# Kernel tuning notes

Measured on AMD Instinct MI355X. Metric: run time of the kernel, lower is better.

Reference implementation:

```python
import jax, jax.numpy as jnp
import numpy as np

B, S, C, H, W = 4, 32, 128, 16, 32
HID = 128
DEPTH = 2


def conv2d_same(x, w, b):
    # x: [B,Cin,H,W], w: [Cout,Cin,3,3] -> [B,Cout,H,W]
    y = jax.lax.conv_general_dilated(x, w, window_strides=(1, 1), padding='SAME',
                                     dimension_numbers=('NCHW', 'OIHW', 'NCHW'))
    return y + b[None, :, None, None]


def setup_inputs() -> dict:
    key = jax.random.key(0)
    ks = jax.random.split(key, 12)
    sc = 0.02
    x = jax.random.normal(ks[0], (B, S, C, H, W), dtype=jnp.float32)
    # stacked ConvLSTM cell params; input to each cell is C==HID channels
    conv_w = sc * jax.random.normal(ks[1], (DEPTH, 4 * HID, C + HID, 3, 3), dtype=jnp.float32)
    conv_b = jnp.zeros((DEPTH, 4 * HID), dtype=jnp.float32)
    init_h = 0.01 * jax.random.normal(ks[2], (DEPTH, HID), dtype=jnp.float32)
    init_c = 0.01 * jax.random.normal(ks[3], (DEPTH, HID), dtype=jnp.float32)
    fc_w = sc * jax.random.normal(ks[4], (C, HID), dtype=jnp.float32)
    fc_b = jnp.zeros((C,), dtype=jnp.float32)
    fco_w = sc * jax.random.normal(ks[5], (1, C), dtype=jnp.float32)
    fco_b = jnp.zeros((1,), dtype=jnp.float32)
    fca_w = sc * jax.random.normal(ks[6], (1, C), dtype=jnp.float32)
    fca_b = jnp.zeros((1,), dtype=jnp.float32)
    return dict(x=x, conv_w=conv_w, conv_b=conv_b, init_h=init_h, init_c=init_c,
                fc_w=fc_w, fc_b=fc_b, fco_w=fco_w, fco_b=fco_b, fca_w=fca_w, fca_b=fca_b)


def _forward(x, conv_w, conv_b, init_h, init_c, fc_w, fc_b, fco_w, fco_b, fca_w, fca_b):
    b, s, c, h, w = x.shape
    hid = init_h.shape[1]
    xs = jnp.moveaxis(x, 1, 0)  # [S,B,C,H,W] time-major for scan
    for d in range(conv_w.shape[0]):  # fixed small depth loop
        wd, bd = conv_w[d], conv_b[d]
        h0 = jnp.broadcast_to(init_h[d][None, :, None, None], (b, hid, h, w))
        c0 = jnp.broadcast_to(init_c[d][None, :, None, None], (b, hid, h, w))

        def step(carry, x_t):
            hs, cs = carry
            z = conv2d_same(jnp.concatenate([x_t, hs], axis=1), wd, bd)
            zi, zf, zg, zo = jnp.split(z, 4, axis=1)  # gate order i,f,g,o
            cs = jax.nn.sigmoid(zf) * cs + jax.nn.sigmoid(zi) * jnp.tanh(zg)
            hs = jax.nn.sigmoid(zo) * jnp.tanh(cs)
            return (hs, cs), hs

        _, xs = jax.lax.scan(step, (h0, c0), xs)
    # global average pool over H,W then heads
    feat = jnp.moveaxis(xs.mean(axis=(3, 4)), 0, 1)  # [B,S,HID]
    feat = jax.nn.relu(feat @ fc_w.T + fc_b)
    offset = feat @ fco_w.T + fco_b  # [B,S,1]
    angle = feat @ fca_w.T + fca_b   # [B,S,1]
    return offset, angle


def reference(x, conv_w, conv_b, init_h, init_c, fc_w, fc_b, fco_w, fco_b, fca_w, fca_b):
    return _forward(x, conv_w, conv_b, init_h, init_c, fc_w, fc_b, fco_w, fco_b, fca_w, fca_b)
```

## Files before the change

### kernel.cpp

```cpp
#include <hip/hip_runtime.h>

#define BB 4
#define SS 32
#define CC 128
#define HH 16
#define WW 32
#define HID 128
#define DEPTH 2
#define CIN 256
#define COUT 512
#define K9 (CIN * 9)
#define KH 1152
#define KFULL (2 * KH)
#define HW (HH * WW)
#define MM (BB * HW)
#define ACT (BB * HW * 128)

typedef __attribute__((ext_vector_type(4))) float f32x4;
typedef __attribute__((ext_vector_type(8))) short bf16x8;

static __device__ __forceinline__ unsigned short f2bf(float f) {
    union { float f; unsigned u; } v; v.f = f;
    unsigned r = v.u + 0x7FFF + ((v.u >> 16) & 1);
    return (unsigned short)(r >> 16);
}
static __device__ __forceinline__ float bf2f(unsigned short h) {
    union { float f; unsigned u; } v; v.u = ((unsigned)h) << 16; return v.f;
}

__global__ void transpose_w_kernel(const float* __restrict__ w,
                                   unsigned short* __restrict__ wh) {
    int idx = blockIdx.x * 256 + threadIdx.x;
    if (idx >= DEPTH * K9 * COUT) return;
    int n = idx % COUT;
    int k = (idx / COUT) % K9;
    int d = idx / (COUT * K9);
    int cin = k / 9, tap = k % 9;
    float v = w[(((long)(d * COUT + n) * CIN + cin) * 9) + tap];
    int row = (cin < CC) ? (tap * CC + cin) : (KH + tap * HID + (cin - CC));
    int g = n >> 7, r = n & 127;
    int ng = (r >> 4) * 64 + g * 16 + (r & 15);
    wh[((long)d * COUT + ng) * KFULL + row] = f2bf(v);
}

__global__ void pack_x_kernel(const float* __restrict__ x,
                              unsigned* __restrict__ xh32) {
    __shared__ unsigned lh[128 * 33];
    const int tid = threadIdx.x;
    const int sb  = blockIdx.x;
    const int s   = sb >> 2;
    const int b   = sb & 3;
    const int hw0 = blockIdx.y * 64;
    const float* src = x + ((long)(b * SS + s) * CC) * HW;

    #pragma unroll
    for (int it = 0; it < 16; ++it) {
        int cc = it * 8 + (tid >> 5);
        int hw = (tid & 31) * 2;
        float2 v = *(const float2*)&src[cc * HW + hw0 + hw];
        unsigned short h0 = f2bf(v.x), h1 = f2bf(v.y);
        lh[cc * 33 + (hw >> 1)] = (unsigned)h0 | ((unsigned)h1 << 16);
    }
    __syncthreads();
    const unsigned short* lhs = (const unsigned short*)lh;
    #pragma unroll
    for (int it = 0; it < 16; ++it) {
        int hw = it * 4 + (tid >> 6);
        int c2 = tid & 63;
        unsigned short a0 = lhs[(2 * c2) * 66 + hw];
        unsigned short a1 = lhs[(2 * c2 + 1) * 66 + hw];
        long o = ((long)sb * HW + hw0 + hw) * 64 + c2;
        xh32[o] = (unsigned)a0 | ((unsigned)a1 << 16);
    }
}

__global__ void init_state_kernel(const float* __restrict__ ih, const float* __restrict__ ic,
                                  unsigned short* __restrict__ hh,
                                  float* __restrict__ c, int d) {
    int idx = blockIdx.x * 256 + threadIdx.x;
    int hid = idx & 127;
    hh[idx] = f2bf(ih[d * HID + hid]);
    c[idx] = ic[d * HID + hid];
}

__global__ void zero_kernel(unsigned* __restrict__ zp) { zp[threadIdx.x] = 0u; }

__launch_bounds__(256)
__global__ void step_dual(
    const unsigned short* __restrict__ x1h, const unsigned short* __restrict__ h1h,
    float* __restrict__ c1, unsigned short* __restrict__ o1h,
    const unsigned short* __restrict__ x2h, const unsigned short* __restrict__ h2h,
    float* __restrict__ c2, unsigned short* __restrict__ o2h,
    const unsigned short* __restrict__ wh,
    const float* __restrict__ bias, const unsigned short* __restrict__ zp,
    int do1, int do2)
{
    __shared__ __align__(16) unsigned short lds[2][8192];

    const int bid  = blockIdx.x;
    const int xcd  = bid & 7;
    const int q    = bid >> 3;
    const int mblk = q & 31;
    const int pp   = xcd + ((q >> 5) << 3);
    const int nblk = pp & 7;
    const int z    = pp >> 3;
    if (z == 0) { if (!do1) return; } else { if (!do2) return; }

    const unsigned short* axh = z ? x2h : x1h;
    const unsigned short* ahh = z ? h2h : h1h;
    const unsigned short* wph = wh + (long)z * COUT * KFULL;
    const float* bsel  = bias + z * COUT;
    float* csel        = z ? c2 : c1;
    unsigned short* ohh = z ? o2h : o1h;

    const int m0   = mblk * 64;
    const int n0g  = nblk * 64;
    const int hid0 = nblk * 16;
    const int tid  = threadIdx.x;
    const int lane = tid & 63;
    const int wv   = tid >> 6;
    const int wm   = (wv >> 1) * 32;
    const int wn   = (wv & 1) * 32;
    const int b    = m0 >> 9;
    const int hwl  = m0 & 511;
    const int y0   = hwl >> 5;

    const int row1 = wv * 16 + (lane >> 3);
    const int row2 = row1 + 8;
    const int jch  = lane & 7;
    const int jx1  = jch ^ (row1 & 7);
    const int jx2  = jch ^ (row2 & 7);
    const int sx1  = row1 & 31, sy1b = row1 >> 5;
    const int sx2  = row2 & 31, sy2b = row2 >> 5;
    const long bhw = (long)b * HW;
    const long bro1 = (long)(n0g + row1) * KFULL + jx1 * 8;
    const long bro2 = (long)(n0g + row2) * KFULL + jx2 * 8;

#define ISSUE(tt, pb) do {                                                        \
        const int _tt = (tt);                                                     \
        const long _k0 = (long)_tt * 64;                                          \
        int _ks = (_tt < 18) ? _tt : _tt - 18;                                    \
        int _tap = _ks >> 1;                                                      \
        int _c0  = (_ks & 1) << 6;                                                \
        int _ky  = _tap / 3 - 1;                                                  \
        int _kx  = _tap - (_tap / 3) * 3 - 1;                                     \
        const unsigned short* _sh = (_tt < 18) ? axh : ahh;                       \
        int _y1 = y0 + sy1b + _ky, _x1 = sx1 + _kx;                               \
        int _y2 = y0 + sy2b + _ky, _x2 = sx2 + _kx;                               \
        bool _o1 = (unsigned)_y1 < (unsigned)HH && (unsigned)_x1 < (unsigned)WW;  \
        bool _o2 = (unsigned)_y2 < (unsigned)HH && (unsigned)_x2 < (unsigned)WW;  \
        long _a1 = ((bhw + _y1 * WW + _x1) << 7) + _c0 + jx1 * 8;                 \
        long _a2 = ((bhw + _y2 * WW + _x2) << 7) + _c0 + jx2 * 8;                 \
        __builtin_amdgcn_global_load_lds(                                         \
            (const unsigned int*)(_o1 ? _sh + _a1 : zp),                          \
            (unsigned int*)&lds[pb][wv * 1024], 16, 0, 0);                        \
        __builtin_amdgcn_global_load_lds(                                         \
            (const unsigned int*)(_o2 ? _sh + _a2 : zp),                          \
            (unsigned int*)&lds[pb][wv * 1024 + 512], 16, 0, 0);                  \
        __builtin_amdgcn_global_load_lds(                                         \
            (const unsigned int*)(wph + bro1 + _k0),                              \
            (unsigned int*)&lds[pb][4096 + wv * 1024], 16, 0, 0);                 \
        __builtin_amdgcn_global_load_lds(                                         \
            (const unsigned int*)(wph + bro2 + _k0),                              \
            (unsigned int*)&lds[pb][4096 + wv * 1024 + 512], 16, 0, 0);           \
    } while (0)

    f32x4 acc00 = (f32x4){0.f,0.f,0.f,0.f};
    f32x4 acc01 = (f32x4){0.f,0.f,0.f,0.f};
    f32x4 acc10 = (f32x4){0.f,0.f,0.f,0.f};
    f32x4 acc11 = (f32x4){0.f,0.f,0.f,0.f};

    const int fr  = lane & 15;
    const int kqi = lane >> 4;
    const int am0 = wm + fr;
    const int am1 = wm + 16 + fr;
    const int bn0 = wn + fr;
    const int bn1 = wn + 16 + fr;

#define COMPUTE(P) do {                                                                  \
        const unsigned short* L = &lds[P][0];                                            \
        __builtin_amdgcn_s_setprio(1);                                                   \
        _Pragma("unroll")                                                                \
        for (int s = 0; s < 2; ++s) {                                                    \
            const int ca = s * 4 + kqi;                                  \
            bf16x8 fa0 = *(const bf16x8*)&L[am0 * 64 + ((ca ^ (am0 & 7)) << 3)];         \
            bf16x8 fa1 = *(const bf16x8*)&L[am1 * 64 + ((ca ^ (am1 & 7)) << 3)];         \
            bf16x8 fb0 = *(const bf16x8*)&L[4096 + bn0 * 64 + ((ca ^ (bn0 & 7)) << 3)];  \
            bf16x8 fb1 = *(const bf16x8*)&L[4096 + bn1 * 64 + ((ca ^ (bn1 & 7)) << 3)];  \
            acc00 = __builtin_amdgcn_mfma_f32_16x16x32_bf16(fa0, fb0, acc00, 0, 0, 0);   \
            acc01 = __builtin_amdgcn_mfma_f32_16x16x32_bf16(fa0, fb1, acc01, 0, 0, 0);   \
            acc10 = __builtin_amdgcn_mfma_f32_16x16x32_bf16(fa1, fb0, acc10, 0, 0, 0);   \
            acc11 = __builtin_amdgcn_mfma_f32_16x16x32_bf16(fa1, fb1, acc11, 0, 0, 0);   \
        }                                                                                \
        __builtin_amdgcn_s_setprio(0);                                                   \
    } while (0)

    ISSUE(0, 0);
    __syncthreads();

    int p = 0;
    for (int tt = 0; tt < 36; ++tt) {
        if (tt + 1 < 36) ISSUE(tt + 1, 1 - p);
        COMPUTE(p);
        __syncthreads();
        p ^= 1;
    }

#undef ISSUE
#undef COMPUTE

    float* zt = (float*)&lds[0][0];
    {
        const int rm = (lane >> 4) * 4;
        const int cn = lane & 15;
        *(float4*)&zt[(wn + cn) * 68 + wm + rm]           = *(float4*)&acc00;
        *(float4*)&zt[(wn + 16 + cn) * 68 + wm + rm]      = *(float4*)&acc01;
        *(float4*)&zt[(wn + cn) * 68 + wm + 16 + rm]      = *(float4*)&acc10;
        *(float4*)&zt[(wn + 16 + cn) * 68 + wm + 16 + rm] = *(float4*)&acc11;
    }
    __syncthreads();

    #pragma unroll
    for (int i2 = 0; i2 < 4; ++i2) {
        int e  = i2 * 256 + tid;
        int m  = e & 63;
        int jh = e >> 6;
        float g4[4];
        #pragma unroll
        for (int gi = 0; gi < 4; ++gi)
            g4[gi] = zt[(gi * 16 + jh) * 68 + m] + bsel[gi * 128 + hid0 + jh];
        long idx = ((long)b * HW + hwl + m) * 128 + hid0 + jh;
        float si = 1.f / (1.f + expf(-g4[0]));
        float sf = 1.f / (1.f + expf(-g4[1]));
        float so = 1.f / (1.f + expf(-g4[3]));
        float cs = sf * csel[idx] + si * tanhf(g4[2]);
        float hs = so * tanhf(cs);
        csel[idx] = cs;
        ohh[idx] = f2bf(hs);
    }
}

__global__ void pool_kernel(const unsigned short* __restrict__ s2h,
                            float* __restrict__ pooled) {
    int bs = blockIdx.x;
    int j  = threadIdx.x;
    const unsigned short* ph = s2h + (long)bs * HW * 128 + j;
    float sum = 0.f;
    #pragma unroll 8
    for (int hw = 0; hw < HW; ++hw)
        sum += bf2f(ph[hw * 128]);
    pooled[bs * HID + j] = sum * (1.f / HW);
}

__global__ void head_kernel(const float* __restrict__ pooled,
                            const float* __restrict__ fc_w, const float* __restrict__ fc_b,
                            const float* __restrict__ fco_w, const float* __restrict__ fco_b,
                            const float* __restrict__ fca_w, const float* __restrict__ fca_b,
                            float* __restrict__ out) {
    int bs = blockIdx.x;
    int b  = bs / SS;
    int s  = bs % SS;
    int j  = threadIdx.x;
    const float* prow = pooled + (long)(s * BB + b) * HID;
    float acc = fc_b[j];
    #pragma unroll 4
    for (int k = 0; k < HID; ++k) acc += fc_w[j * HID + k] * prow[k];
    float f = fmaxf(acc, 0.f);
    __shared__ float ro[128], ra[128];
    ro[j] = f * fco_w[j];
    ra[j] = f * fca_w[j];
    __syncthreads();
    for (int off = 64; off; off >>= 1) {
        if (j < off) { ro[j] += ro[j + off]; ra[j] += ra[j + off]; }
        __syncthreads();
    }
    if (j == 0) {
        out[bs]           = ro[0] + fco_b[0];
        out[BB * SS + bs] = ra[0] + fca_b[0];
    }
}

extern "C" void kernel_launch(void* const* d_in, const int* in_sizes, int n_in,
                              void* d_out, int out_size, void* d_ws, size_t ws_size,
                              hipStream_t stream) {
    const float* x      = (const float*)d_in[0];
    const float* conv_w = (const float*)d_in[1];
    const float* conv_b = (const float*)d_in[2];
    const float* init_h = (const float*)d_in[3];
    const float* init_c = (const float*)d_in[4];
    const float* fc_w   = (const float*)d_in[5];
    const float* fc_b   = (const float*)d_in[6];
    const float* fco_w  = (const float*)d_in[7];
    const float* fco_b  = (const float*)d_in[8];
    const float* fca_w  = (const float*)d_in[9];
    const float* fca_b  = (const float*)d_in[10];
    float* out = (float*)d_out;

    unsigned short* wh  = (unsigned short*)d_ws;
    unsigned short* xph = wh  + (long)DEPTH * COUT * KFULL;
    unsigned short* s1h = xph + (long)SS * ACT;
    unsigned short* s2h = s1h + (long)SS * ACT;
    unsigned short* h1h = s2h + (long)SS * ACT;
    unsigned short* h2h = h1h + ACT;
    float* c1     = (float*)(h2h + ACT);
    float* c2     = c1 + ACT;
    float* pooled = c2 + ACT;
    unsigned short* zp = (unsigned short*)(pooled + SS * BB * HID);

    transpose_w_kernel<<<(DEPTH * K9 * COUT + 255) / 256, 256, 0, stream>>>(conv_w, wh);
    pack_x_kernel<<<dim3(SS * BB, HW / 64), 256, 0, stream>>>(x, (unsigned*)xph);
    init_state_kernel<<<ACT / 256, 256, 0, stream>>>(init_h, init_c, h1h, c1, 0);
    init_state_kernel<<<ACT / 256, 256, 0, stream>>>(init_h, init_c, h2h, c2, 1);
    zero_kernel<<<1, 64, 0, stream>>>((unsigned*)zp);

    for (int t = 0; t <= SS; ++t) {
        int do1 = (t < SS) ? 1 : 0;
        int do2 = (t >= 1) ? 1 : 0;
        int t1 = (t < SS) ? t : SS - 1;
        int u2 = (t >= 1) ? t - 1 : 0;
        const unsigned short* ax1h = xph + (long)t1 * ACT;
        const unsigned short* ah1h = (t1 == 0) ? h1h : s1h + (long)(t1 - 1) * ACT;
        unsigned short* ao1h = s1h + (long)t1 * ACT;
        const unsigned short* ax2h = s1h + (long)u2 * ACT;
        const unsigned short* ah2h = (u2 == 0) ? h2h : s2h + (long)(u2 - 1) * ACT;
        unsigned short* ao2h = s2h + (long)u2 * ACT;
        step_dual<<<512, 256, 0, stream>>>(
            ax1h, ah1h, c1, ao1h,
            ax2h, ah2h, c2, ao2h,
            wh, conv_b, zp, do1, do2);
    }

    pool_kernel<<<SS * BB, 128, 0, stream>>>(s2h, pooled);
    head_kernel<<<BB * SS, 128, 0, stream>>>(pooled, fc_w, fc_b, fco_w, fco_b, fca_w, fca_b, out);
}
```

Before: 862.9 us.

## Double K-tile depth to 128 and vectorize the gate epilogue stores

```diff
diff --git a/kernel.cpp b/kernel.cpp
--- a/kernel.cpp
+++ b/kernel.cpp
@@ -95,7 +95,7 @@
     const float* __restrict__ bias, const unsigned short* __restrict__ zp,
     int do1, int do2)
 {
-    __shared__ __align__(16) unsigned short lds[2][8192];
+    __shared__ __align__(16) unsigned short lds[2][16384];
 
     const int bid  = blockIdx.x;
     const int xcd  = bid & 7;
@@ -124,45 +124,39 @@
     const int b    = m0 >> 9;
     const int hwl  = m0 & 511;
     const int y0   = hwl >> 5;
-
-    const int row1 = wv * 16 + (lane >> 3);
-    const int row2 = row1 + 8;
-    const int jch  = lane & 7;
-    const int jx1  = jch ^ (row1 & 7);
-    const int jx2  = jch ^ (row2 & 7);
-    const int sx1  = row1 & 31, sy1b = row1 >> 5;
-    const int sx2  = row2 & 31, sy2b = row2 >> 5;
     const long bhw = (long)b * HW;
-    const long bro1 = (long)(n0g + row1) * KFULL + jx1 * 8;
-    const long bro2 = (long)(n0g + row2) * KFULL + jx2 * 8;
+
+    int sy_[4], sx_[4], ax_[4];
+    long bro_[4];
+    #pragma unroll
+    for (int s = 0; s < 4; ++s) {
+        int row = wv * 16 + s * 4 + (lane >> 4);
+        int jx  = (lane & 15) ^ (row & 7);
+        sx_[s] = row & 31;
+        sy_[s] = y0 + (row >> 5);
+        ax_[s] = jx * 8;
+        bro_[s] = (long)(n0g + row) * KFULL + jx * 8;
+    }
 
 #define ISSUE(tt, pb) do {                                                        \
         const int _tt = (tt);                                                     \
-        const long _k0 = (long)_tt * 64;                                          \
-        int _ks = (_tt < 18) ? _tt : _tt - 18;                                    \
-        int _tap = _ks >> 1;                                                      \
-        int _c0  = (_ks & 1) << 6;                                                \
-        int _ky  = _tap / 3 - 1;                                                  \
-        int _kx  = _tap - (_tap / 3) * 3 - 1;                                     \
-        const unsigned short* _sh = (_tt < 18) ? axh : ahh;                       \
-        int _y1 = y0 + sy1b + _ky, _x1 = sx1 + _kx;                               \
-        int _y2 = y0 + sy2b + _ky, _x2 = sx2 + _kx;                               \
-        bool _o1 = (unsigned)_y1 < (unsigned)HH && (unsigned)_x1 < (unsigned)WW;  \
-        bool _o2 = (unsigned)_y2 < (unsigned)HH && (unsigned)_x2 < (unsigned)WW;  \
-        long _a1 = ((bhw + _y1 * WW + _x1) << 7) + _c0 + jx1 * 8;                 \
-        long _a2 = ((bhw + _y2 * WW + _x2) << 7) + _c0 + jx2 * 8;                 \
-        __builtin_amdgcn_global_load_lds(                                         \
-            (const unsigned int*)(_o1 ? _sh + _a1 : zp),                          \
-            (unsigned int*)&lds[pb][wv * 1024], 16, 0, 0);                        \
-        __builtin_amdgcn_global_load_lds(                                         \
-            (const unsigned int*)(_o2 ? _sh + _a2 : zp),                          \
-            (unsigned int*)&lds[pb][wv * 1024 + 512], 16, 0, 0);                  \
-        __builtin_amdgcn_global_load_lds(                                         \
-            (const unsigned int*)(wph + bro1 + _k0),                              \
-            (unsigned int*)&lds[pb][4096 + wv * 1024], 16, 0, 0);                 \
-        __builtin_amdgcn_global_load_lds(                                         \
-            (const unsigned int*)(wph + bro2 + _k0),                              \
-            (unsigned int*)&lds[pb][4096 + wv * 1024 + 512], 16, 0, 0);           \
+        const int _tap = (_tt < 9) ? _tt : _tt - 9;                               \
+        const unsigned short* _sh = (_tt < 9) ? axh : ahh;                        \
+        const int _ky = _tap / 3 - 1;                                             \
+        const int _kx = _tap - (_tap / 3) * 3 - 1;                                \
+        const long _bk = (long)_tt * 128;                                         \
+        _Pragma("unroll")                                                         \
+        for (int _s = 0; _s < 4; ++_s) {                                          \
+            int _yy = sy_[_s] + _ky, _xq = sx_[_s] + _kx;                         \
+            bool _ok = (unsigned)_yy < (unsigned)HH && (unsigned)_xq < (unsigned)WW;\
+            long _a = ((bhw + _yy * WW + _xq) << 7) + ax_[_s];                    \
+            __builtin_amdgcn_global_load_lds(                                     \
+                (const unsigned int*)(_ok ? _sh + _a : zp),                       \
+                (unsigned int*)&lds[pb][wv * 2048 + _s * 512], 16, 0, 0);         \
+            __builtin_amdgcn_global_load_lds(                                     \
+                (const unsigned int*)(wph + bro_[_s] + _bk),                      \
+                (unsigned int*)&lds[pb][8192 + wv * 2048 + _s * 512], 16, 0, 0);  \
+        }                                                                         \
     } while (0)
 
     f32x4 acc00 = (f32x4){0.f,0.f,0.f,0.f};
@@ -177,30 +171,30 @@
     const int bn0 = wn + fr;
     const int bn1 = wn + 16 + fr;
 
-#define COMPUTE(P) do {                                                                  \
-        const unsigned short* L = &lds[P][0];                                            \
-        __builtin_amdgcn_s_setprio(1);                                                   \
-        _Pragma("unroll")                                                                \
-        for (int s = 0; s < 2; ++s) {                                                    \
-            const int ca = s * 4 + kqi;                                  \
-            bf16x8 fa0 = *(const bf16x8*)&L[am0 * 64 + ((ca ^ (am0 & 7)) << 3)];         \
-            bf16x8 fa1 = *(const bf16x8*)&L[am1 * 64 + ((ca ^ (am1 & 7)) << 3)];         \
-            bf16x8 fb0 = *(const bf16x8*)&L[4096 + bn0 * 64 + ((ca ^ (bn0 & 7)) << 3)];  \
-            bf16x8 fb1 = *(const bf16x8*)&L[4096 + bn1 * 64 + ((ca ^ (bn1 & 7)) << 3)];  \
-            acc00 = __builtin_amdgcn_mfma_f32_16x16x32_bf16(fa0, fb0, acc00, 0, 0, 0);   \
-            acc01 = __builtin_amdgcn_mfma_f32_16x16x32_bf16(fa0, fb1, acc01, 0, 0, 0);   \
-            acc10 = __builtin_amdgcn_mfma_f32_16x16x32_bf16(fa1, fb0, acc10, 0, 0, 0);   \
-            acc11 = __builtin_amdgcn_mfma_f32_16x16x32_bf16(fa1, fb1, acc11, 0, 0, 0);   \
-        }                                                                                \
-        __builtin_amdgcn_s_setprio(0);                                                   \
+#define COMPUTE(P) do {                                                                   \
+        const unsigned short* L = &lds[P][0];                                             \
+        __builtin_amdgcn_s_setprio(1);                                                    \
+        _Pragma("unroll")                                                                 \
+        for (int s2 = 0; s2 < 4; ++s2) {                                                  \
+            const int ca = s2 * 4 + kqi;                                 \
+            bf16x8 fa0 = *(const bf16x8*)&L[am0 * 128 + ((ca ^ (am0 & 7)) << 3)];         \
+            bf16x8 fa1 = *(const bf16x8*)&L[am1 * 128 + ((ca ^ (am1 & 7)) << 3)];         \
+            bf16x8 fb0 = *(const bf16x8*)&L[8192 + bn0 * 128 + ((ca ^ (bn0 & 7)) << 3)];  \
+            bf16x8 fb1 = *(const bf16x8*)&L[8192 + bn1 * 128 + ((ca ^ (bn1 & 7)) << 3)];  \
+            acc00 = __builtin_amdgcn_mfma_f32_16x16x32_bf16(fa0, fb0, acc00, 0, 0, 0);    \
+            acc01 = __builtin_amdgcn_mfma_f32_16x16x32_bf16(fa0, fb1, acc01, 0, 0, 0);    \
+            acc10 = __builtin_amdgcn_mfma_f32_16x16x32_bf16(fa1, fb0, acc10, 0, 0, 0);    \
+            acc11 = __builtin_amdgcn_mfma_f32_16x16x32_bf16(fa1, fb1, acc11, 0, 0, 0);    \
+        }                                                                                 \
+        __builtin_amdgcn_s_setprio(0);                                                    \
     } while (0)
 
     ISSUE(0, 0);
     __syncthreads();
 
     int p = 0;
-    for (int tt = 0; tt < 36; ++tt) {
-        if (tt + 1 < 36) ISSUE(tt + 1, 1 - p);
+    for (int tt = 0; tt < 18; ++tt) {
+        if (tt + 1 < 18) ISSUE(tt + 1, 1 - p);
         COMPUTE(p);
         __syncthreads();
         p ^= 1;
@@ -220,23 +214,34 @@
     }
     __syncthreads();
 
-    #pragma unroll
-    for (int i2 = 0; i2 < 4; ++i2) {
-        int e  = i2 * 256 + tid;
-        int m  = e & 63;
-        int jh = e >> 6;
-        float g4[4];
+    {
+        const int m    = tid & 63;
+        const int jset = tid >> 6;
+        float g[4][4];
         #pragma unroll
-        for (int gi = 0; gi < 4; ++gi)
-            g4[gi] = zt[(gi * 16 + jh) * 68 + m] + bsel[gi * 128 + hid0 + jh];
-        long idx = ((long)b * HW + hwl + m) * 128 + hid0 + jh;
-        float si = 1.f / (1.f + expf(-g4[0]));
-        float sf = 1.f / (1.f + expf(-g4[1]));
-        float so = 1.f / (1.f + expf(-g4[3]));
-        float cs = sf * csel[idx] + si * tanhf(g4[2]);
-        float hs = so * tanhf(cs);
-        csel[idx] = cs;
-        ohh[idx] = f2bf(hs);
+        for (int ji = 0; ji < 4; ++ji) {
+            int jh = jset * 4 + ji;
+            #pragma unroll
+            for (int gi = 0; gi < 4; ++gi)
+                g[ji][gi] = zt[(gi * 16 + jh) * 68 + m] + bsel[gi * 128 + hid0 + jh];
+        }
+        long base = ((long)b * HW + hwl + m) * 128 + hid0 + jset * 4;
+        f32x4 cv = *(const f32x4*)&csel[base];
+        float hv[4];
+        #pragma unroll
+        for (int ji = 0; ji < 4; ++ji) {
+            float si = 1.f / (1.f + expf(-g[ji][0]));
+            float sf = 1.f / (1.f + expf(-g[ji][1]));
+            float so = 1.f / (1.f + expf(-g[ji][3]));
+            float cs = sf * cv[ji] + si * tanhf(g[ji][2]);
+            cv[ji] = cs;
+            hv[ji] = so * tanhf(cs);
+        }
+        *(f32x4*)&csel[base] = cv;
+        uint2 hp;
+        hp.x = (unsigned)f2bf(hv[0]) | ((unsigned)f2bf(hv[1]) << 16);
+        hp.y = (unsigned)f2bf(hv[2]) | ((unsigned)f2bf(hv[3]) << 16);
+        *(uint2*)&ohh[base] = hp;
     }
 }
 
```

After: 697.6 us, median of 2. -19.2%, faster.
